# Kernel tuning notes

Measured on AMD Instinct MI355X. Metric: run time of the kernel, lower is better.

## Reference

```python
import jax, jax.numpy as jnp
import numpy as np

B, C_IN, H, W = 16, 16, 64, 64
C_OUT, KH, KW, DH, DW = 16, 3, 3, 1, 1
OH = (H - KH) // DH + 1  # 62
OW = (W - KW) // DW + 1  # 62


def setup_inputs() -> dict:
    key = jax.random.key(0)
    k1, k2 = jax.random.split(key)
    x = jax.random.normal(k1, (B, C_IN, H, W), dtype=jnp.float32)
    weight = jax.random.normal(k2, (1, C_OUT, C_IN, OH, OW, KH * KW), dtype=jnp.float32)
    return {"x": x, "weight": weight}


def _extract_patches(x):
    # Equivalent to torch unfold(2,kh,dh).unfold(3,kw,dw).view(..., kh*kw):
    # patches[b,c,y,x,k] with k = i*KW + j (row-major over kernel window).
    slabs = [x[:, :, i:i + OH * DH:DH, j:j + OW * DW:DW]
             for i in range(KH) for j in range(KW)]
    return jnp.stack(slabs, axis=-1)  # [B, C_IN, OH, OW, KH*KW]


def reference(x, weight):
    patches = _extract_patches(x)
    # out[b,o,y,x] = sum_{c,k} patches[b,c,y,x,k] * weight[0,o,c,y,x,k]
    out = jnp.einsum('bcyxk,ocyxk->boyx', patches, weight[0])
    return out
```

## Files before the change

kernel.cpp:

```cpp
#include <hip/hip_runtime.h>


#define CIN   16
#define COUT  16
#define HH    64
#define WW    64
#define OHH   62
#define OWW   62

#define WOSTR (CIN * OHH * OWW * 9)
#define WCSTR (OHH * OWW * 9)
#define OROW  388

__device__ __forceinline__ int ldsIdx(int o, int xi, int k) {
    int j = k >> 2;
    int p = (j + xi) % 3;
    return o * OROW + xi * 12 + p * 4 + (k & 3);
}

__global__ __launch_bounds__(256, 1)
void lc2d(const float* __restrict__ xg,
          const float* __restrict__ wg,
          float* __restrict__ outg)
{
    __shared__ float Wl[8 * OROW];

    const int tid = threadIdx.x;
    const int y   = blockIdx.x;
    const int xh  = blockIdx.y;
    const int oh  = blockIdx.z;
    const int x0  = xh * 32;
    const int nx  = xh ? (OWW - 32) : 32;
    const int M   = nx * 9 / 2;
    const int tot = 8 * M;

    const int xl  = tid & 31;
    const int og  = (tid >> 5) & 1;
    const int bg  = tid >> 6;
    const int pos = x0 + xl;
    const bool valid = pos < OWW;
    const int xp  = valid ? pos : (OWW - 1);

    int st_o[5], st_fo[5];
    bool st_en[5];
    #pragma unroll
    for (int r = 0; r < 5; ++r) {
        int id = tid + 256 * r;
        st_en[r] = id < tot;
        int idc = st_en[r] ? id : 0;
        int o = idc / M;
        st_o[r]  = o;
        st_fo[r] = 2 * (idc - o * M);
    }

    const float* wbase = wg + (size_t)oh * 8 * WOSTR + (size_t)(y * OWW + x0) * 9;

    float2 pf[5];
    #pragma unroll
    for (int r = 0; r < 5; ++r)
        if (st_en[r])
            pf[r] = *(const float2*)(wbase + (size_t)st_o[r] * WOSTR + st_fo[r]);
    #pragma unroll
    for (int r = 0; r < 5; ++r) {
        if (st_en[r]) {
            int fo = st_fo[r];
            int xi = fo / 9;
            int k  = fo - xi * 9;
            Wl[ldsIdx(st_o[r], xi, k)] = pf[r].x;
            int xi2 = (k == 8) ? xi + 1 : xi;
            int k2  = (k == 8) ? 0 : k + 1;
            Wl[ldsIdx(st_o[r], xi2, k2)] = pf[r].y;
        }
    }
    __syncthreads();

    float acc[4][4];
    #pragma unroll
    for (int t = 0; t < 4; ++t)
        #pragma unroll
        for (int b = 0; b < 4; ++b) acc[t][b] = 0.f;

    const float* xbb = xg + (size_t)y * WW + xp;

    for (int c = 0; c < CIN; ++c) {
        float2 npf[5];
        if (c + 1 < CIN) {
            #pragma unroll
            for (int r = 0; r < 5; ++r)
                if (st_en[r])
                    npf[r] = *(const float2*)(wbase + (size_t)st_o[r] * WOSTR
                                              + (size_t)(c + 1) * WCSTR + st_fo[r]);
        }

        float xv[4][9];
        #pragma unroll
        for (int b = 0; b < 4; ++b) {
            const float* xr = xbb + (size_t)(bg * 4 + b) * (CIN * HH * WW)
                                  + (size_t)c * (HH * WW);
            #pragma unroll
            for (int i = 0; i < 3; ++i)
                #pragma unroll
                for (int j = 0; j < 3; ++j)
                    xv[b][i * 3 + j] = xr[i * WW + j];
        }

        #pragma unroll
        for (int t = 0; t < 4; ++t) {
            const int lo   = og * 4 + t;
            const int base = lo * OROW + xl * 12;
            const int p0   = xl % 3;
            const float4 w0 = *(const float4*)&Wl[base + p0 * 4];
            const float4 w1 = *(const float4*)&Wl[base + ((p0 + 1) % 3) * 4];
            const float  w8 = Wl[base + ((p0 + 2) % 3) * 4];
            #pragma unroll
            for (int b = 0; b < 4; ++b) {
                float s = acc[t][b];
                s = fmaf(w0.x, xv[b][0], s);
                s = fmaf(w0.y, xv[b][1], s);
                s = fmaf(w0.z, xv[b][2], s);
                s = fmaf(w0.w, xv[b][3], s);
                s = fmaf(w1.x, xv[b][4], s);
                s = fmaf(w1.y, xv[b][5], s);
                s = fmaf(w1.z, xv[b][6], s);
                s = fmaf(w1.w, xv[b][7], s);
                s = fmaf(w8,   xv[b][8], s);
                acc[t][b] = s;
            }
        }

        if (c + 1 < CIN) {
            __syncthreads();
            #pragma unroll
            for (int r = 0; r < 5; ++r) {
                if (st_en[r]) {
                    int fo = st_fo[r];
                    int xi = fo / 9;
                    int k  = fo - xi * 9;
                    Wl[ldsIdx(st_o[r], xi, k)] = npf[r].x;
                    int xi2 = (k == 8) ? xi + 1 : xi;
                    int k2  = (k == 8) ? 0 : k + 1;
                    Wl[ldsIdx(st_o[r], xi2, k2)] = npf[r].y;
                }
            }
            __syncthreads();
        }
    }

    if (valid) {
        #pragma unroll
        for (int t = 0; t < 4; ++t) {
            const int o = oh * 8 + og * 4 + t;
            #pragma unroll
            for (int b = 0; b < 4; ++b) {
                const int bb = bg * 4 + b;
                outg[((size_t)(bb * COUT + o) * OHH + y) * OWW + pos] = acc[t][b];
            }
        }
    }
}

extern "C" void kernel_launch(void* const* d_in, const int* in_sizes, int n_in,
                              void* d_out, int out_size, void* d_ws, size_t ws_size,
                              hipStream_t stream) {
    const float* x = (const float*)d_in[0];
    const float* w = (const float*)d_in[1];
    float* out = (float*)d_out;

    dim3 grid(OHH, 2, 2);
    dim3 block(256);
    lc2d<<<grid, block, 0, stream>>>(x, w, out);
}
```

Baseline: 90.65 us.

## Double-buffer LDS weights and double block size with fewer batches per thread

Moves to 512-thread blocks. Each thread now handles 2 batches instead of 4 (bg ranges over 8 groups), and the per-thread weight staging loads drop from 5 to 3. The weight tile in shared memory is double-buffered, which removes one __syncthreads per channel iteration, and the LDS write indices are precomputed once. The aim is more parallel waves to hide the weight streaming latency and less barrier overhead, at the cost of fewer FMAs per weight load and twice the LDS footprint.

```diff
diff --git a/kernel.cpp b/kernel.cpp
--- a/kernel.cpp
+++ b/kernel.cpp
@@ -18,12 +18,12 @@
     return o * OROW + xi * 12 + p * 4 + (k & 3);
 }
 
-__global__ __launch_bounds__(256, 1)
+__global__ __launch_bounds__(512, 1)
 void lc2d(const float* __restrict__ xg,
           const float* __restrict__ wg,
           float* __restrict__ outg)
 {
-    __shared__ float Wl[8 * OROW];
+    __shared__ float Wl[2][8 * OROW];
 
     const int tid = threadIdx.x;
     const int y   = blockIdx.x;
@@ -41,79 +41,94 @@
     const bool valid = pos < OWW;
     const int xp  = valid ? pos : (OWW - 1);
 
-    int st_o[5], st_fo[5];
-    bool st_en[5];
+    int st_o[3], st_fo[3];
+    bool st_en[3];
     #pragma unroll
-    for (int r = 0; r < 5; ++r) {
-        int id = tid + 256 * r;
+    for (int r = 0; r < 3; ++r) {
+        int id = tid + 512 * r;
         st_en[r] = id < tot;
         int idc = st_en[r] ? id : 0;
         int o = idc / M;
         st_o[r]  = o;
         st_fo[r] = 2 * (idc - o * M);
     }
+    int wr0[3], wr1[3];
+    #pragma unroll
+    for (int r = 0; r < 3; ++r) {
+        int fo = st_fo[r];
+        int xi = fo / 9;
+        int k  = fo - xi * 9;
+        wr0[r] = ldsIdx(st_o[r], xi, k);
+        int xi2 = (k == 8) ? xi + 1 : xi;
+        int k2  = (k == 8) ? 0 : k + 1;
+        wr1[r] = ldsIdx(st_o[r], xi2, k2);
+    }
 
     const float* wbase = wg + (size_t)oh * 8 * WOSTR + (size_t)(y * OWW + x0) * 9;
 
-    float2 pf[5];
-    #pragma unroll
-    for (int r = 0; r < 5; ++r)
-        if (st_en[r])
-            pf[r] = *(const float2*)(wbase + (size_t)st_o[r] * WOSTR + st_fo[r]);
-    #pragma unroll
-    for (int r = 0; r < 5; ++r) {
-        if (st_en[r]) {
-            int fo = st_fo[r];
-            int xi = fo / 9;
-            int k  = fo - xi * 9;
-            Wl[ldsIdx(st_o[r], xi, k)] = pf[r].x;
-            int xi2 = (k == 8) ? xi + 1 : xi;
-            int k2  = (k == 8) ? 0 : k + 1;
-            Wl[ldsIdx(st_o[r], xi2, k2)] = pf[r].y;
+    {
+        float2 pf[3];
+        #pragma unroll
+        for (int r = 0; r < 3; ++r)
+            if (st_en[r])
+                pf[r] = *(const float2*)(wbase + (size_t)st_o[r] * WOSTR + st_fo[r]);
+        #pragma unroll
+        for (int r = 0; r < 3; ++r) {
+            if (st_en[r]) {
+                Wl[0][wr0[r]] = pf[r].x;
+                Wl[0][wr1[r]] = pf[r].y;
+            }
         }
     }
     __syncthreads();
 
-    float acc[4][4];
+    float acc[4][2];
     #pragma unroll
-    for (int t = 0; t < 4; ++t)
-        #pragma unroll
-        for (int b = 0; b < 4; ++b) acc[t][b] = 0.f;
+    for (int t = 0; t < 4; ++t) {
+        acc[t][0] = 0.f; acc[t][1] = 0.f;
+    }
 
-    const float* xbb = xg + (size_t)y * WW + xp;
+    const float* xb0 = xg + ((size_t)(bg * 2 + 0) * CIN) * (HH * WW) + (size_t)y * WW + xp;
+    const float* xb1 = xg + ((size_t)(bg * 2 + 1) * CIN) * (HH * WW) + (size_t)y * WW + xp;
+
+    const int p0 = (xl % 3) * 4;
+    const int p1 = ((xl + 1) % 3) * 4;
+    const int p2 = ((xl + 2) % 3) * 4;
 
     for (int c = 0; c < CIN; ++c) {
-        float2 npf[5];
+        const float* cur = Wl[c & 1];
+        float*       nxt = Wl[(c + 1) & 1];
+
+        float2 npf[3];
         if (c + 1 < CIN) {
             #pragma unroll
-            for (int r = 0; r < 5; ++r)
+            for (int r = 0; r < 3; ++r)
                 if (st_en[r])
                     npf[r] = *(const float2*)(wbase + (size_t)st_o[r] * WOSTR
                                               + (size_t)(c + 1) * WCSTR + st_fo[r]);
         }
 
-        float xv[4][9];
-        #pragma unroll
-        for (int b = 0; b < 4; ++b) {
-            const float* xr = xbb + (size_t)(bg * 4 + b) * (CIN * HH * WW)
-                                  + (size_t)c * (HH * WW);
+        float xv[2][9];
+        {
+            const float* xr0 = xb0 + (size_t)c * (HH * WW);
+            const float* xr1 = xb1 + (size_t)c * (HH * WW);
             #pragma unroll
             for (int i = 0; i < 3; ++i)
                 #pragma unroll
-                for (int j = 0; j < 3; ++j)
-                    xv[b][i * 3 + j] = xr[i * WW + j];
+                for (int j = 0; j < 3; ++j) {
+                    xv[0][i * 3 + j] = xr0[i * WW + j];
+                    xv[1][i * 3 + j] = xr1[i * WW + j];
+                }
         }
 
         #pragma unroll
         for (int t = 0; t < 4; ++t) {
-            const int lo   = og * 4 + t;
-            const int base = lo * OROW + xl * 12;
-            const int p0   = xl % 3;
-            const float4 w0 = *(const float4*)&Wl[base + p0 * 4];
-            const float4 w1 = *(const float4*)&Wl[base + ((p0 + 1) % 3) * 4];
-            const float  w8 = Wl[base + ((p0 + 2) % 3) * 4];
+            const int base = (og * 4 + t) * OROW + xl * 12;
+            const float4 w0 = *(const float4*)&cur[base + p0];
+            const float4 w1 = *(const float4*)&cur[base + p1];
+            const float  w8 = cur[base + p2];
             #pragma unroll
-            for (int b = 0; b < 4; ++b) {
+            for (int b = 0; b < 2; ++b) {
                 float s = acc[t][b];
                 s = fmaf(w0.x, xv[b][0], s);
                 s = fmaf(w0.y, xv[b][1], s);
@@ -129,17 +144,11 @@
         }
 
         if (c + 1 < CIN) {
-            __syncthreads();
             #pragma unroll
-            for (int r = 0; r < 5; ++r) {
+            for (int r = 0; r < 3; ++r) {
                 if (st_en[r]) {
-                    int fo = st_fo[r];
-                    int xi = fo / 9;
-                    int k  = fo - xi * 9;
-                    Wl[ldsIdx(st_o[r], xi, k)] = npf[r].x;
-                    int xi2 = (k == 8) ? xi + 1 : xi;
-                    int k2  = (k == 8) ? 0 : k + 1;
-                    Wl[ldsIdx(st_o[r], xi2, k2)] = npf[r].y;
+                    nxt[wr0[r]] = npf[r].x;
+                    nxt[wr1[r]] = npf[r].y;
                 }
             }
             __syncthreads();
@@ -151,8 +160,8 @@
         for (int t = 0; t < 4; ++t) {
             const int o = oh * 8 + og * 4 + t;
             #pragma unroll
-            for (int b = 0; b < 4; ++b) {
-                const int bb = bg * 4 + b;
+            for (int b = 0; b < 2; ++b) {
+                const int bb = bg * 2 + b;
                 outg[((size_t)(bb * COUT + o) * OHH + y) * OWW + pos] = acc[t][b];
             }
         }
@@ -167,6 +176,6 @@
     float* out = (float*)d_out;
 
     dim3 grid(OHH, 2, 2);
-    dim3 block(256);
+    dim3 block(512);
     lc2d<<<grid, block, 0, stream>>>(x, w, out);
 }
```

After: 89.12 us. About the same (-1.7%).

## Split input channels across blocks with atomic accumulation and double-buffered LDS

Applied to the files above, without the earlier changes.

Splits the 16 input channels into two halves handled by separate blocks, which doubles the grid, and accumulates partial sums into the output with atomicAdd after a separate zeroing kernel. It also replaces the staggered float2 LDS layout with a simpler transposed per-tap layout that is double-buffered, so only one barrier is needed per channel. Occupancy is raised to 2 blocks per CU. The aim is more parallelism to hide the latency of streaming the large weight tensor, at the cost of an extra launch, atomic traffic, and uncoalesced 9-float weight loads per thread.

```diff
diff --git a/kernel.cpp b/kernel.cpp
--- a/kernel.cpp
+++ b/kernel.cpp
@@ -7,32 +7,32 @@
 #define WW    64
 #define OHH   62
 #define OWW   62
+#define HW    (HH * WW)
 
 #define WOSTR (CIN * OHH * OWW * 9)
 #define WCSTR (OHH * OWW * 9)
-#define OROW  388
+#define NC    8
+#define OTILE 288
 
-__device__ __forceinline__ int ldsIdx(int o, int xi, int k) {
-    int j = k >> 2;
-    int p = (j + xi) % 3;
-    return o * OROW + xi * 12 + p * 4 + (k & 3);
+__global__ __launch_bounds__(256)
+void zero_out(float* __restrict__ outg) {
+    ((float4*)outg)[blockIdx.x * 256 + threadIdx.x] = make_float4(0.f, 0.f, 0.f, 0.f);
 }
 
-__global__ __launch_bounds__(256, 1)
+__global__ __launch_bounds__(256, 2)
 void lc2d(const float* __restrict__ xg,
           const float* __restrict__ wg,
           float* __restrict__ outg)
 {
-    __shared__ float Wl[8 * OROW];
+    __shared__ float Wl[2][8 * OTILE];
 
     const int tid = threadIdx.x;
     const int y   = blockIdx.x;
     const int xh  = blockIdx.y;
-    const int oh  = blockIdx.z;
+    const int oh  = blockIdx.z & 1;
+    const int ch  = blockIdx.z >> 1;
     const int x0  = xh * 32;
-    const int nx  = xh ? (OWW - 32) : 32;
-    const int M   = nx * 9 / 2;
-    const int tot = 8 * M;
+    const int cstart = ch * NC;
 
     const int xl  = tid & 31;
     const int og  = (tid >> 5) & 1;
@@ -41,36 +41,19 @@
     const bool valid = pos < OWW;
     const int xp  = valid ? pos : (OWW - 1);
 
-    int st_o[5], st_fo[5];
-    bool st_en[5];
-    #pragma unroll
-    for (int r = 0; r < 5; ++r) {
-        int id = tid + 256 * r;
-        st_en[r] = id < tot;
-        int idc = st_en[r] ? id : 0;
-        int o = idc / M;
-        st_o[r]  = o;
-        st_fo[r] = 2 * (idc - o * M);
-    }
+    const int q   = tid >> 5;
+    const int sxi = tid & 31;
+    const int sx  = (x0 + sxi < OWW) ? (x0 + sxi) : (OWW - 1);
+    const float* wst = wg + (size_t)(oh * 8 + q) * WOSTR + (size_t)cstart * WCSTR
+                          + (size_t)(y * OWW + sx) * 9;
+    const int wrbase = q * OTILE + sxi;
 
-    const float* wbase = wg + (size_t)oh * 8 * WOSTR + (size_t)(y * OWW + x0) * 9;
-
-    float2 pf[5];
-    #pragma unroll
-    for (int r = 0; r < 5; ++r)
-        if (st_en[r])
-            pf[r] = *(const float2*)(wbase + (size_t)st_o[r] * WOSTR + st_fo[r]);
-    #pragma unroll
-    for (int r = 0; r < 5; ++r) {
-        if (st_en[r]) {
-            int fo = st_fo[r];
-            int xi = fo / 9;
-            int k  = fo - xi * 9;
-            Wl[ldsIdx(st_o[r], xi, k)] = pf[r].x;
-            int xi2 = (k == 8) ? xi + 1 : xi;
-            int k2  = (k == 8) ? 0 : k + 1;
-            Wl[ldsIdx(st_o[r], xi2, k2)] = pf[r].y;
-        }
+    {
+        float pf[9];
+        #pragma unroll
+        for (int r = 0; r < 9; ++r) pf[r] = wst[r];
+        #pragma unroll
+        for (int r = 0; r < 9; ++r) Wl[0][wrbase + r * 32] = pf[r];
     }
     __syncthreads();
 
@@ -80,23 +63,17 @@
         #pragma unroll
         for (int b = 0; b < 4; ++b) acc[t][b] = 0.f;
 
-    const float* xbb = xg + (size_t)y * WW + xp;
+    const float* xbb = xg + ((size_t)(bg * 4) * CIN + cstart) * HW
+                          + (size_t)y * WW + xp;
 
-    for (int c = 0; c < CIN; ++c) {
-        float2 npf[5];
-        if (c + 1 < CIN) {
-            #pragma unroll
-            for (int r = 0; r < 5; ++r)
-                if (st_en[r])
-                    npf[r] = *(const float2*)(wbase + (size_t)st_o[r] * WOSTR
-                                              + (size_t)(c + 1) * WCSTR + st_fo[r]);
-        }
+    for (int cc = 0; cc < NC; ++cc) {
+        const float* cur = Wl[cc & 1];
+        float*       nxt = Wl[(cc + 1) & 1];
 
         float xv[4][9];
         #pragma unroll
         for (int b = 0; b < 4; ++b) {
-            const float* xr = xbb + (size_t)(bg * 4 + b) * (CIN * HH * WW)
-                                  + (size_t)c * (HH * WW);
+            const float* xr = xbb + ((size_t)b * CIN + cc) * HW;
             #pragma unroll
             for (int i = 0; i < 3; ++i)
                 #pragma unroll
@@ -104,44 +81,32 @@
                     xv[b][i * 3 + j] = xr[i * WW + j];
         }
 
+        float pf[9];
+        if (cc + 1 < NC) {
+            const float* ws = wst + (size_t)(cc + 1) * WCSTR;
+            #pragma unroll
+            for (int r = 0; r < 9; ++r) pf[r] = ws[r];
+        }
+
         #pragma unroll
         for (int t = 0; t < 4; ++t) {
-            const int lo   = og * 4 + t;
-            const int base = lo * OROW + xl * 12;
-            const int p0   = xl % 3;
-            const float4 w0 = *(const float4*)&Wl[base + p0 * 4];
-            const float4 w1 = *(const float4*)&Wl[base + ((p0 + 1) % 3) * 4];
-            const float  w8 = Wl[base + ((p0 + 2) % 3) * 4];
+            const float* wb = &cur[(og * 4 + t) * OTILE + xl];
+            float wv[9];
+            #pragma unroll
+            for (int k = 0; k < 9; ++k) wv[k] = wb[k * 32];
             #pragma unroll
             for (int b = 0; b < 4; ++b) {
                 float s = acc[t][b];
-                s = fmaf(w0.x, xv[b][0], s);
-                s = fmaf(w0.y, xv[b][1], s);
-                s = fmaf(w0.z, xv[b][2], s);
-                s = fmaf(w0.w, xv[b][3], s);
-                s = fmaf(w1.x, xv[b][4], s);
-                s = fmaf(w1.y, xv[b][5], s);
-                s = fmaf(w1.z, xv[b][6], s);
-                s = fmaf(w1.w, xv[b][7], s);
-                s = fmaf(w8,   xv[b][8], s);
+                #pragma unroll
+                for (int k = 0; k < 9; ++k)
+                    s = fmaf(wv[k], xv[b][k], s);
                 acc[t][b] = s;
             }
         }
 
-        if (c + 1 < CIN) {
-            __syncthreads();
+        if (cc + 1 < NC) {
             #pragma unroll
-            for (int r = 0; r < 5; ++r) {
-                if (st_en[r]) {
-                    int fo = st_fo[r];
-                    int xi = fo / 9;
-                    int k  = fo - xi * 9;
-                    Wl[ldsIdx(st_o[r], xi, k)] = npf[r].x;
-                    int xi2 = (k == 8) ? xi + 1 : xi;
-                    int k2  = (k == 8) ? 0 : k + 1;
-                    Wl[ldsIdx(st_o[r], xi2, k2)] = npf[r].y;
-                }
-            }
+            for (int r = 0; r < 9; ++r) nxt[wrbase + r * 32] = pf[r];
             __syncthreads();
         }
     }
@@ -153,7 +118,8 @@
             #pragma unroll
             for (int b = 0; b < 4; ++b) {
                 const int bb = bg * 4 + b;
-                outg[((size_t)(bb * COUT + o) * OHH + y) * OWW + pos] = acc[t][b];
+                atomicAdd(&outg[((size_t)(bb * COUT + o) * OHH + y) * OWW + pos],
+                          acc[t][b]);
             }
         }
     }
@@ -166,7 +132,7 @@
     const float* w = (const float*)d_in[1];
     float* out = (float*)d_out;
 
-    dim3 grid(OHH, 2, 2);
-    dim3 block(256);
-    lc2d<<<grid, block, 0, stream>>>(x, w, out);
+    zero_out<<<dim3(961), dim3(256), 0, stream>>>(out);
+    dim3 grid(OHH, 2, 4);
+    lc2d<<<grid, dim3(256), 0, stream>>>(x, w, out);
 }
```

After: 94.32 us. 4.1% more time.
